# Optimization experiments

Measured on AMD Instinct MI355X. Metric: run time of the kernel, lower is better.

## Reference

```python
import jax, jax.numpy as jnp
import numpy as np

IN_DIM = 256
HIDDEN = 256
N_TAPES = 2
DIM = HIDDEN // N_TAPES          # 128
LSTM_H = 8 * N_TAPES             # 16
SEQ = 256
BATCH = 32
TAPELEN = 256


def setup_inputs() -> dict:
    key = jax.random.key(0)
    ks = jax.random.split(key, 10)
    s = 0.05
    inputs = jax.random.normal(ks[0], (SEQ, BATCH, IN_DIM), jnp.float32)
    # LSTM params (torch gate order: i, f, g, o)
    W_ih = s * jax.random.normal(ks[1], (4 * LSTM_H, IN_DIM), jnp.float32)
    W_hh = s * jax.random.normal(ks[2], (4 * LSTM_H, LSTM_H), jnp.float32)
    b_ih = s * jax.random.normal(ks[3], (4 * LSTM_H,), jnp.float32)
    b_hh = s * jax.random.normal(ks[4], (4 * LSTM_H,), jnp.float32)
    # value / out linear layers
    W_val = s * jax.random.normal(ks[5], (HIDDEN, IN_DIM), jnp.float32)
    b_val = s * jax.random.normal(ks[6], (HIDDEN,), jnp.float32)
    W_out = s * jax.random.normal(ks[7], (HIDDEN, HIDDEN), jnp.float32)
    b_out = s * jax.random.normal(ks[8], (HIDDEN,), jnp.float32)
    return {
        'inputs': inputs, 'tapelen': TAPELEN,
        'W_ih': W_ih, 'W_hh': W_hh, 'b_ih': b_ih, 'b_hh': b_hh,
        'W_val': W_val, 'b_val': b_val, 'W_out': W_out, 'b_out': b_out,
    }


def _lstm(inputs, W_ih, W_hh, b_ih, b_hh):
    # inputs: [S, B, in_dim] -> hidden seq [S, B, LSTM_H], torch gate order i,f,g,o
    S, B, _ = inputs.shape
    xg = inputs @ W_ih.T + (b_ih + b_hh)  # precompute input contribution [S,B,4H]

    def step(carry, xt):
        h, c = carry
        g = xt + h @ W_hh.T
        i, f, gg, o = jnp.split(g, 4, axis=-1)
        c = jax.nn.sigmoid(f) * c + jax.nn.sigmoid(i) * jnp.tanh(gg)
        h = jax.nn.sigmoid(o) * jnp.tanh(c)
        return (h, c), h

    h0 = jnp.zeros((B, W_hh.shape[1]), inputs.dtype)
    (_, _), hs = jax.lax.scan(step, (h0, h0), xg)
    return hs


def reference(inputs, tapelen, W_ih, W_hh, b_ih, b_hh, W_val, b_val, W_out, b_out):
    seqlen, bs, _ = inputs.shape
    values = (inputs @ W_val.T + b_val).reshape(seqlen, bs, N_TAPES, DIM)

    actions = _lstm(inputs, W_ih, W_hh, b_ih, b_hh).reshape(seqlen, bs, N_TAPES, 8)
    dirs_r = jax.nn.softmax(actions[..., 0:3], axis=-1)
    dirs_w = jax.nn.softmax(actions[..., 3:6], axis=-1)
    rwprobs = jax.nn.sigmoid(actions[..., 6:8])

    tape0 = jnp.zeros((tapelen, bs, N_TAPES, DIM), inputs.dtype)
    pos0 = jnp.zeros((tapelen, bs, N_TAPES), inputs.dtype).at[0].set(1.0)

    def step(carry, xs):
        tape, rpos, wpos = carry
        v, rd, wd, rw = xs  # v:[B,T,C] rd/wd:[B,T,3] rw:[B,T,2]
        # write: replace value at soft write position, gated by rw[...,1]
        oldval = jnp.einsum('lntc,lnt->ntc', tape, wpos)
        newmem = jnp.einsum('lnt,ntc->lntc', wpos, v - oldval)
        tape = tape + newmem * rw[None, :, :, 1:2]
        # NOTE: faithful to source — write-position shifts roll rpos, not wpos
        next_w = jnp.roll(rpos, 1, axis=0)
        prev_w = jnp.roll(rpos, -1, axis=0)
        wpos = prev_w * wd[None, :, :, 0] + wpos * wd[None, :, :, 1] + next_w * wd[None, :, :, 2]
        # read, gated by rw[...,0]
        read_out = jnp.einsum('lntc,lnt->ntc', tape, rpos * rw[None, :, :, 0])
        next_r = jnp.roll(rpos, 1, axis=0)
        prev_r = jnp.roll(rpos, -1, axis=0)
        rpos = prev_r * rd[None, :, :, 0] + rpos * rd[None, :, :, 1] + next_r * rd[None, :, :, 2]
        return (tape, rpos, wpos), read_out

    (tape, rpos, wpos), reads = jax.lax.scan(
        step, (tape0, pos0, pos0), (values, dirs_r, dirs_w, rwprobs))

    outputs = reads.reshape(seqlen, bs, HIDDEN) @ W_out.T + b_out
    return outputs, tape, (rpos, wpos)
```

## Files before the change

kernel.cpp:

```cpp
#include <hip/hip_runtime.h>

#define SEQ    256
#define BATCH  32
#define NT     2
#define DIM    128
#define LTAPE  256

typedef float f32x4 __attribute__((ext_vector_type(4)));
typedef short s16x8 __attribute__((ext_vector_type(8)));
typedef unsigned int u32;
typedef unsigned short u16;

__device__ __forceinline__ float sigm(float x) { return 1.f / (1.f + __expf(-x)); }
__device__ __forceinline__ float tanh_(float x) { float e = __expf(2.f * x); return 1.f - 2.f / (e + 1.f); }
__device__ __forceinline__ u16 f2bf(float x) {
  u32 u = __builtin_bit_cast(u32, x);
  u32 r = (u + 0x7fffu + ((u >> 16) & 1u)) >> 16;
  return (u16)r;
}
__device__ __forceinline__ float bf2f(u16 b) {
  u32 u = ((u32)b) << 16; return __builtin_bit_cast(float, u);
}

template<bool A_BF16, bool OUT_BF16>
__global__ __launch_bounds__(256) void gemm_mfma(
    const void* __restrict__ Av, const float* __restrict__ W,
    const float* __restrict__ bias, void* __restrict__ Cv, int N) {
  __shared__ u16 As[128 * 40];
  __shared__ u16 Bs[64 * 40];
  const int tid = threadIdx.x;
  const int bm = blockIdx.x * 128, bn = blockIdx.y * 64;
  const int wv = tid >> 6, lane = tid & 63;
  const int wm = wv >> 1, wn = wv & 1;
  const int l15 = lane & 15, l4 = lane >> 4;
  f32x4 acc[4][2] = {};
  const int arow = tid >> 1, ahalf = tid & 1;
  const int brow = (tid & 127) >> 1, bhalf = tid & 1;

  for (int k0 = 0; k0 < 256; k0 += 32) {
    u16 abuf[16];
    if (A_BF16) {
      const u16* A = (const u16*)Av;
      const uint4* p = (const uint4*)(A + (size_t)(bm + arow) * 256 + k0 + ahalf * 16);
      *(uint4*)(abuf) = p[0]; *(uint4*)(abuf + 8) = p[1];
    } else {
      const float* A = (const float*)Av;
      const float* src = A + (size_t)(bm + arow) * 256 + k0 + ahalf * 16;
      float4 x0 = ((const float4*)src)[0], x1 = ((const float4*)src)[1];
      float4 x2 = ((const float4*)src)[2], x3 = ((const float4*)src)[3];
      float xs[16] = {x0.x, x0.y, x0.z, x0.w, x1.x, x1.y, x1.z, x1.w,
                      x2.x, x2.y, x2.z, x2.w, x3.x, x3.y, x3.z, x3.w};
#pragma unroll
      for (int j = 0; j < 16; ++j) abuf[j] = f2bf(xs[j]);
    }
    u16 bbuf[16];
    if (tid < 128) {
      const float* src = W + (size_t)(bn + brow) * 256 + k0 + bhalf * 16;
      float4 x0 = ((const float4*)src)[0], x1 = ((const float4*)src)[1];
      float4 x2 = ((const float4*)src)[2], x3 = ((const float4*)src)[3];
      float xs[16] = {x0.x, x0.y, x0.z, x0.w, x1.x, x1.y, x1.z, x1.w,
                      x2.x, x2.y, x2.z, x2.w, x3.x, x3.y, x3.z, x3.w};
#pragma unroll
      for (int j = 0; j < 16; ++j) bbuf[j] = f2bf(xs[j]);
    }
    __syncthreads();
    *(uint4*)&As[arow * 40 + ahalf * 16] = *(const uint4*)(abuf);
    *(uint4*)&As[arow * 40 + ahalf * 16 + 8] = *(const uint4*)(abuf + 8);
    if (tid < 128) {
      *(uint4*)&Bs[brow * 40 + bhalf * 16] = *(const uint4*)(bbuf);
      *(uint4*)&Bs[brow * 40 + bhalf * 16 + 8] = *(const uint4*)(bbuf + 8);
    }
    __syncthreads();
    s16x8 af[4], bfr[2];
#pragma unroll
    for (int mi = 0; mi < 4; ++mi)
      af[mi] = *(const s16x8*)&As[(wm * 64 + mi * 16 + l15) * 40 + l4 * 8];
#pragma unroll
    for (int ni = 0; ni < 2; ++ni)
      bfr[ni] = *(const s16x8*)&Bs[(wn * 32 + ni * 16 + l15) * 40 + l4 * 8];
#pragma unroll
    for (int mi = 0; mi < 4; ++mi)
#pragma unroll
      for (int ni = 0; ni < 2; ++ni)
        acc[mi][ni] = __builtin_amdgcn_mfma_f32_16x16x32_bf16(af[mi], bfr[ni], acc[mi][ni], 0, 0, 0);
  }
#pragma unroll
  for (int mi = 0; mi < 4; ++mi)
#pragma unroll
    for (int ni = 0; ni < 2; ++ni)
#pragma unroll
      for (int r = 0; r < 4; ++r) {
        int row = bm + wm * 64 + mi * 16 + l4 * 4 + r;
        int col = bn + wn * 32 + ni * 16 + l15;
        float val = acc[mi][ni][r] + bias[col];
        if (OUT_BF16) ((u16*)Cv)[(size_t)row * N + col] = f2bf(val);
        else          ((float*)Cv)[(size_t)row * N + col] = val;
      }
}

__global__ __launch_bounds__(256) void gemm_nt(
    const float* __restrict__ A, const float* __restrict__ W,
    const float* __restrict__ b1, const float* __restrict__ b2,
    float* __restrict__ C, int N) {
  __shared__ float Asm[16][68];
  __shared__ float Bsm[16][68];
  const int tid = threadIdx.x;
  const int bm = blockIdx.x * 64;
  const int bn = blockIdx.y * 64;
  const int lr = tid >> 2;
  const int lc4 = (tid & 3) * 4;
  const int tm = (tid & 15) * 4;
  const int tn = (tid >> 4) * 4;
  float acc[4][4];
#pragma unroll
  for (int i = 0; i < 4; ++i)
#pragma unroll
    for (int j = 0; j < 4; ++j) acc[i][j] = 0.f;
  for (int k0 = 0; k0 < 256; k0 += 16) {
    float4 av = *reinterpret_cast<const float4*>(&A[(bm + lr) * 256 + k0 + lc4]);
    float4 bv = *reinterpret_cast<const float4*>(&W[(bn + lr) * 256 + k0 + lc4]);
    __syncthreads();
    Asm[lc4 + 0][lr] = av.x; Asm[lc4 + 1][lr] = av.y; Asm[lc4 + 2][lr] = av.z; Asm[lc4 + 3][lr] = av.w;
    Bsm[lc4 + 0][lr] = bv.x; Bsm[lc4 + 1][lr] = bv.y; Bsm[lc4 + 2][lr] = bv.z; Bsm[lc4 + 3][lr] = bv.w;
    __syncthreads();
#pragma unroll
    for (int kk = 0; kk < 16; ++kk) {
      float4 a = *reinterpret_cast<const float4*>(&Asm[kk][tm]);
      float4 b = *reinterpret_cast<const float4*>(&Bsm[kk][tn]);
      float a_[4] = {a.x, a.y, a.z, a.w};
      float b_[4] = {b.x, b.y, b.z, b.w};
#pragma unroll
      for (int i = 0; i < 4; ++i)
#pragma unroll
        for (int j = 0; j < 4; ++j) acc[i][j] += a_[i] * b_[j];
    }
  }
#pragma unroll
  for (int i = 0; i < 4; ++i)
#pragma unroll
    for (int j = 0; j < 4; ++j) {
      int n = bn + tn + j;
      float bias = b1[n] + (b2 ? b2[n] : 0.f);
      C[(size_t)(bm + tm + i) * N + n] = acc[i][j] + bias;
    }
}

__global__ __launch_bounds__(64, 1) void lstm_kernel(
    const float* __restrict__ xg,
    const float* __restrict__ W_hh,
    float* __restrict__ hout) {
  const int lane = threadIdx.x;
  const int b = blockIdx.x;
  const int k = lane & 15, q = lane >> 4;
  float w[16];
#pragma unroll
  for (int kk = 0; kk < 16; ++kk) w[kk] = W_hh[lane * 16 + kk];
  float h = 0.f, c = 0.f;
  const float* xb = xg + (size_t)b * 64 + lane;
  float xA = xb[0 * 2048];
  float xB = xb[1 * 2048];
  float xC = xb[2 * 2048];
  float xD = xb[3 * 2048];

#define LSTM_STEP(S, XV)                                                     \
  {                                                                          \
    float hb[16];                                                            \
    _Pragma("unroll") for (int kk = 0; kk < 16; ++kk)                        \
      hb[kk] = __shfl(h, kk, 64);                                            \
    float pa = w[0] * hb[0], pb = w[1] * hb[1];                              \
    float pcc = w[2] * hb[2], pd = w[3] * hb[3];                             \
    _Pragma("unroll") for (int kk = 4; kk < 16; kk += 4) {                   \
      pa += w[kk + 0] * hb[kk + 0];                                         \
      pb += w[kk + 1] * hb[kk + 1];                                         \
      pcc += w[kk + 2] * hb[kk + 2];                                        \
      pd += w[kk + 3] * hb[kk + 3];                                         \
    }                                                                        \
    float g = XV + (pa + pb) + (pcc + pd);                                   \
    float gi = __shfl(g, k, 64);                                             \
    float gf = __shfl(g, 16 + k, 64);                                        \
    float gg = __shfl(g, 32 + k, 64);                                        \
    float go = __shfl(g, 48 + k, 64);                                        \
    c = sigm(gf) * c + sigm(gi) * tanh_(gg);                                 \
    h = sigm(go) * tanh_(c);                                                 \
    if (q == 0) hout[(size_t)((S) * 32 + b) * 16 + k] = h;                   \
  }

  for (int s0 = 0; s0 < SEQ; s0 += 4) {
    int p4 = s0 + 4; if (p4 > 255) p4 = 255;
    int p5 = s0 + 5; if (p5 > 255) p5 = 255;
    int p6 = s0 + 6; if (p6 > 255) p6 = 255;
    int p7 = s0 + 7; if (p7 > 255) p7 = 255;
    float nA = xb[(size_t)p4 * 2048];
    float nB = xb[(size_t)p5 * 2048];
    float nC = xb[(size_t)p6 * 2048];
    float nD = xb[(size_t)p7 * 2048];
    LSTM_STEP(s0 + 0, xA);
    LSTM_STEP(s0 + 1, xB);
    LSTM_STEP(s0 + 2, xC);
    LSTM_STEP(s0 + 3, xD);
    xA = nA; xB = nB; xC = nC; xD = nD;
  }
#undef LSTM_STEP
}

__global__ __launch_bounds__(256) void head_kernel(
    const float* __restrict__ hout,
    float* __restrict__ pc) {
  const int idx = blockIdx.x * 256 + threadIdx.x;
  const int e = idx & 7, s = (idx >> 3) & 255, p = idx >> 11;
  const int b = p >> 1, t = p & 1;
  const float* hp = hout + ((size_t)(s * 32 + b)) * 16 + t * 8;
  float outv;
  if (e < 3) {
    float a0 = hp[0], a1 = hp[1], a2 = hp[2];
    float m = fmaxf(a0, fmaxf(a1, a2));
    float e0 = __expf(a0 - m), e1 = __expf(a1 - m), e2 = __expf(a2 - m);
    float inv = 1.f / (e0 + e1 + e2);
    outv = (e == 0 ? e0 : (e == 1 ? e1 : e2)) * inv;
  } else if (e < 6) {
    float a3 = hp[3], a4 = hp[4], a5 = hp[5];
    float m = fmaxf(a3, fmaxf(a4, a5));
    float e0 = __expf(a3 - m), e1 = __expf(a4 - m), e2 = __expf(a5 - m);
    float inv = 1.f / (e0 + e1 + e2);
    outv = (e == 3 ? e0 : (e == 4 ? e1 : e2)) * inv;
  } else {
    outv = sigm(hp[e]);
  }
  pc[idx] = outv;
}

__global__ __launch_bounds__(64, 1) void pos_kernel(
    const float* __restrict__ pc,
    float* __restrict__ posW, float* __restrict__ posRs,
    float* __restrict__ out_rpos, float* __restrict__ out_wpos) {
  const int p = blockIdx.x, lane = threadIdx.x;
  float r0 = 0, r1 = 0, r2 = 0, r3 = 0, w0 = 0, w1 = 0, w2 = 0, w3 = 0;
  if (lane == 0) { r0 = 1.f; w0 = 1.f; }
  const float* pcb = pc + (size_t)p * 2048;
  float4 c0 = *(const float4*)&pcb[0];
  float4 c1 = *(const float4*)&pcb[4];
  for (int s0 = 0; s0 < SEQ; s0 += 4) {
    float4 pf[8];
#pragma unroll
    for (int u = 0; u < 4; ++u) {
      int sn = s0 + u + 1; if (sn > 255) sn = 255;
      pf[2 * u]     = *(const float4*)&pcb[sn * 8];
      pf[2 * u + 1] = *(const float4*)&pcb[sn * 8 + 4];
    }
#pragma unroll
    for (int u = 0; u < 4; ++u) {
      const int s = s0 + u;
      size_t ob = ((size_t)p * 256 + s) * 256 + lane * 4;
      *(float4*)(posW + ob) = make_float4(w0, w1, w2, w3);
      float rw0 = c1.z;
      *(float4*)(posRs + ob) = make_float4(r0 * rw0, r1 * rw0, r2 * rw0, r3 * rw0);
      const float crd0 = c0.x, crd1 = c0.y, crd2 = c0.z;
      const float cwd0 = c0.w, cwd1 = c1.x, cwd2 = c1.y;
      float rn  = __shfl(r0, (lane + 1) & 63, 64);
      float rpv = __shfl(r3, (lane + 63) & 63, 64);
      float nw0 = r1 * cwd0 + w0 * cwd1 + rpv * cwd2;
      float nr0 = r1 * crd0 + r0 * crd1 + rpv * crd2;
      float nw1 = r2 * cwd0 + w1 * cwd1 + r0 * cwd2;
      float nr1 = r2 * crd0 + r1 * crd1 + r0 * crd2;
      float nw2 = r3 * cwd0 + w2 * cwd1 + r1 * cwd2;
      float nr2 = r3 * crd0 + r2 * crd1 + r1 * crd2;
      float nw3 = rn * cwd0 + w3 * cwd1 + r2 * cwd2;
      float nr3 = rn * crd0 + r3 * crd1 + r2 * crd2;
      r0 = nr0; r1 = nr1; r2 = nr2; r3 = nr3;
      w0 = nw0; w1 = nw1; w2 = nw2; w3 = nw3;
      c0 = pf[2 * u]; c1 = pf[2 * u + 1];
    }
  }
  out_rpos[(size_t)(lane * 4 + 0) * 64 + p] = r0;
  out_rpos[(size_t)(lane * 4 + 1) * 64 + p] = r1;
  out_rpos[(size_t)(lane * 4 + 2) * 64 + p] = r2;
  out_rpos[(size_t)(lane * 4 + 3) * 64 + p] = r3;
  out_wpos[(size_t)(lane * 4 + 0) * 64 + p] = w0;
  out_wpos[(size_t)(lane * 4 + 1) * 64 + p] = w1;
  out_wpos[(size_t)(lane * 4 + 2) * 64 + p] = w2;
  out_wpos[(size_t)(lane * 4 + 3) * 64 + p] = w3;
}

template<bool TRANS_A, bool B_NT, int MODE, int OUTK, int BROW>
__global__ __launch_bounds__(256) void bgemm(
    const float* __restrict__ A, const float* __restrict__ B,
    const float* __restrict__ pc, float* __restrict__ C,
    size_t sA, size_t sB) {
  __shared__ u16 Ah[128 * 40], Al[128 * 40], Bh[64 * 40], Bl[64 * 40];
  const int p = blockIdx.z;
  const int bm = blockIdx.y * 128, bn = blockIdx.x * 64;
  const int tid = threadIdx.x, wv = tid >> 6, lane = tid & 63;
  const int wm = wv >> 1, wn = wv & 1, l15 = lane & 15, l4 = lane >> 4;
  const int b = p >> 1, t = p & 1;

  if (MODE == 1 && bn >= bm + 128) return;
  if (MODE == 2 && bn >= bm + 128) {
#pragma unroll
    for (int mi = 0; mi < 4; ++mi)
#pragma unroll
      for (int ni = 0; ni < 2; ++ni)
#pragma unroll
        for (int r = 0; r < 4; ++r) {
          int row = bm + wm * 64 + mi * 16 + l4 * 4 + r;
          int col = bn + wn * 32 + ni * 16 + l15;
          C[(size_t)p * 65536 + (size_t)row * 256 + col] = 0.f;
        }
    return;
  }

  const float* Ap = A + (size_t)p * sA;
  const float* Bp = B + (size_t)p * sB;
  f32x4 acc[4][2] = {};

  for (int k0 = 0; k0 < 256; k0 += 32) {
    float xa[16];
    if (!TRANS_A) {
      const int m = tid >> 1, kq = (tid & 1) * 16;
      const float* src = Ap + (size_t)(bm + m) * 256 + k0 + kq;
#pragma unroll
      for (int j = 0; j < 4; ++j) *(float4*)(xa + j * 4) = ((const float4*)src)[j];
    } else {
      const int kr = tid >> 3, mq = (tid & 7) * 16;
      const float* src = Ap + (size_t)(k0 + kr) * 256 + bm + mq;
#pragma unroll
      for (int j = 0; j < 4; ++j) *(float4*)(xa + j * 4) = ((const float4*)src)[j];
    }
    u16 ah[16], al[16];
#pragma unroll
    for (int j = 0; j < 16; ++j) {
      u16 hh = f2bf(xa[j]);
      ah[j] = hh; al[j] = f2bf(xa[j] - bf2f(hh));
    }
    float xb[8];
    if (B_NT) {
      const int n = tid >> 2, kq = (tid & 3) * 8;
      const float* src = Bp + (size_t)(bn + n) * 256 + k0 + kq;
      *(float4*)(xb) = ((const float4*)src)[0];
      *(float4*)(xb + 4) = ((const float4*)src)[1];
    } else {
      const int kr = tid >> 3, nq = (tid & 7) * 8;
      const float* src = Bp + (size_t)(k0 + kr) * BROW + bn + nq;
      *(float4*)(xb) = ((const float4*)src)[0];
      *(float4*)(xb + 4) = ((const float4*)src)[1];
    }
    u16 bh[8], bl[8];
#pragma unroll
    for (int j = 0; j < 8; ++j) {
      u16 hh = f2bf(xb[j]);
      bh[j] = hh; bl[j] = f2bf(xb[j] - bf2f(hh));
    }
    __syncthreads();
    if (!TRANS_A) {
      const int m = tid >> 1, kq = (tid & 1) * 16;
      *(uint4*)&Ah[m * 40 + kq]     = *(const uint4*)(ah);
      *(uint4*)&Ah[m * 40 + kq + 8] = *(const uint4*)(ah + 8);
      *(uint4*)&Al[m * 40 + kq]     = *(const uint4*)(al);
      *(uint4*)&Al[m * 40 + kq + 8] = *(const uint4*)(al + 8);
    } else {
      const int kr = tid >> 3, mq = (tid & 7) * 16;
#pragma unroll
      for (int j = 0; j < 16; ++j) {
        Ah[(mq + j) * 40 + kr] = ah[j];
        Al[(mq + j) * 40 + kr] = al[j];
      }
    }
    if (B_NT) {
      const int n = tid >> 2, kq = (tid & 3) * 8;
      *(uint4*)&Bh[n * 40 + kq] = *(const uint4*)(bh);
      *(uint4*)&Bl[n * 40 + kq] = *(const uint4*)(bl);
    } else {
      const int kr = tid >> 3, nq = (tid & 7) * 8;
#pragma unroll
      for (int j = 0; j < 8; ++j) {
        Bh[(nq + j) * 40 + kr] = bh[j];
        Bl[(nq + j) * 40 + kr] = bl[j];
      }
    }
    __syncthreads();
    s16x8 fah[4], fal[4], fbh[2], fbl[2];
#pragma unroll
    for (int mi = 0; mi < 4; ++mi) {
      fah[mi] = *(const s16x8*)&Ah[(wm * 64 + mi * 16 + l15) * 40 + l4 * 8];
      fal[mi] = *(const s16x8*)&Al[(wm * 64 + mi * 16 + l15) * 40 + l4 * 8];
    }
#pragma unroll
    for (int ni = 0; ni < 2; ++ni) {
      fbh[ni] = *(const s16x8*)&Bh[(wn * 32 + ni * 16 + l15) * 40 + l4 * 8];
      fbl[ni] = *(const s16x8*)&Bl[(wn * 32 + ni * 16 + l15) * 40 + l4 * 8];
    }
#pragma unroll
    for (int mi = 0; mi < 4; ++mi)
#pragma unroll
      for (int ni = 0; ni < 2; ++ni) {
        acc[mi][ni] = __builtin_amdgcn_mfma_f32_16x16x32_bf16(fah[mi], fbh[ni], acc[mi][ni], 0, 0, 0);
        acc[mi][ni] = __builtin_amdgcn_mfma_f32_16x16x32_bf16(fah[mi], fbl[ni], acc[mi][ni], 0, 0, 0);
        acc[mi][ni] = __builtin_amdgcn_mfma_f32_16x16x32_bf16(fal[mi], fbh[ni], acc[mi][ni], 0, 0, 0);
      }
  }
#pragma unroll
  for (int mi = 0; mi < 4; ++mi)
#pragma unroll
    for (int ni = 0; ni < 2; ++ni)
#pragma unroll
      for (int r = 0; r < 4; ++r) {
        int row = bm + wm * 64 + mi * 16 + l4 * 4 + r;
        int col = bn + wn * 32 + ni * 16 + l15;
        float v = acc[mi][ni][r];
        if (MODE == 1) v = (col < row) ? v * pc[((size_t)p * 256 + row) * 8 + 7] : 0.f;
        if (MODE == 2) v = (col <= row) ? v : 0.f;
        if (OUTK == 0)      C[(size_t)p * 65536 + (size_t)row * 256 + col] = v;
        else if (OUTK == 1) C[((size_t)(row * 32 + b)) * 256 + t * 128 + col] = v;
        else                C[((size_t)row * 64 + p) * 128 + col] = v;
      }
}

__global__ __launch_bounds__(64) void inv_kernel(
    const float* __restrict__ L,
    u16* __restrict__ MgH, u16* __restrict__ MgL) {
  const int pk = blockIdx.x;
  const int p = pk >> 3, s0 = (pk & 7) * 32;
  const int lane = threadIdx.x;
  __shared__ float Db[32][33];
  __shared__ float Ms[32][33];
  const float* Lp = L + (size_t)p * 65536;
  {
    const int r = lane >> 1, c0 = (lane & 1) * 16;
    const float* src = Lp + (size_t)(s0 + r) * 256 + s0 + c0;
    float4 v0 = ((const float4*)src)[0], v1 = ((const float4*)src)[1];
    float4 v2 = ((const float4*)src)[2], v3 = ((const float4*)src)[3];
    *(float4*)&Db[r][c0]      = v0; *(float4*)&Db[r][c0 + 4]  = v1;
    *(float4*)&Db[r][c0 + 8]  = v2; *(float4*)&Db[r][c0 + 12] = v3;
  }
  __syncthreads();
  if (lane < 32) {
    const int j = lane;
    float m[32];
#pragma unroll
    for (int r = 0; r < 32; ++r) {
      float xa = (r == j) ? 1.f : 0.f;
      float xb = 0.f;
#pragma unroll
      for (int q = 0; q < 32; ++q) {
        if (q < r) {
          if (q & 1) xb -= Db[r][q] * m[q];
          else       xa -= Db[r][q] * m[q];
        }
      }
      float x = xa + xb;
      m[r] = x;
      Ms[r][j] = x;
    }
  }
  __syncthreads();
  const int l15 = lane & 15, l4 = lane >> 4;
#pragma unroll
  for (int rt = 0; rt < 2; ++rt) {
    u32 wh[4], wl[4];
#pragma unroll
    for (int i2 = 0; i2 < 4; ++i2) {
      float v0 = Ms[rt * 16 + l15][l4 * 8 + i2 * 2];
      float v1 = Ms[rt * 16 + l15][l4 * 8 + i2 * 2 + 1];
      u16 h0 = f2bf(v0), h1 = f2bf(v1);
      u16 g0 = f2bf(v0 - bf2f(h0)), g1 = f2bf(v1 - bf2f(h1));
      wh[i2] = (u32)h0 | ((u32)h1 << 16);
      wl[i2] = (u32)g0 | ((u32)g1 << 16);
    }
    size_t off = (((size_t)pk * 2 + rt) * 64 + lane) * 8;
    *(uint4*)(MgH + off) = make_uint4(wh[0], wh[1], wh[2], wh[3]);
    *(uint4*)(MgL + off) = make_uint4(wl[0], wl[1], wl[2], wl[3]);
  }
}

__global__ __launch_bounds__(256, 1) void solve_kernel(
    const float* __restrict__ L,
    const u16* __restrict__ values,
    const float* __restrict__ pc,
    const u16* __restrict__ MgH, const u16* __restrict__ MgL,
    float* __restrict__ delta) {
  const int p = blockIdx.x >> 1, hf = blockIdx.x & 1;
  const int b = p >> 1, t = p & 1;
  const int tid = threadIdx.x, w = tid >> 6, lane = tid & 63;
  const int l15 = lane & 15, l4 = lane >> 4;
  const int col = w * 16 + l15;
  __shared__ u16 dBsH[64][264];
  __shared__ u16 dBsL[64][264];
  __shared__ u16 Lh[32][264];
  __shared__ u16 Ll[32][264];
  __shared__ u16 accTH[64][40];
  __shared__ u16 accTL[64][40];
  const float* Lp = L + (size_t)p * 65536;
  const int srow = tid >> 3, sseg = tid & 7;

  for (int k = 0; k < 8; ++k) {
    const int s0 = k * 32;
    f32x4 acc0 = {}, acc1 = {};
#pragma unroll
    for (int r = 0; r < 4; ++r) {
      int s = s0 + l4 * 4 + r;
      float rv = bf2f(values[((size_t)(s * 32 + b)) * 256 + t * 128 + hf * 64 + col]);
      acc0[r] = rv * pc[((size_t)p * 256 + s) * 8 + 7];
      int s2 = s + 16;
      float rv2 = bf2f(values[((size_t)(s2 * 32 + b)) * 256 + t * 128 + hf * 64 + col]);
      acc1[r] = rv2 * pc[((size_t)p * 256 + s2) * 8 + 7];
    }
    size_t mo0 = (((size_t)(p * 8 + k) * 2 + 0) * 64 + lane) * 8;
    size_t mo1 = (((size_t)(p * 8 + k) * 2 + 1) * 64 + lane) * 8;
    s16x8 mh0 = *(const s16x8*)(MgH + mo0);
    s16x8 mh1 = *(const s16x8*)(MgH + mo1);
    s16x8 ml0 = *(const s16x8*)(MgL + mo0);
    s16x8 ml1 = *(const s16x8*)(MgL + mo1);
    for (int c4 = sseg; c4 * 4 < s0; c4 += 8) {
      float4 lv = *(const float4*)(Lp + (size_t)(s0 + srow) * 256 + c4 * 4);
      float x0 = -lv.x, x1 = -lv.y, x2 = -lv.z, x3 = -lv.w;
      u16 h0 = f2bf(x0), h1 = f2bf(x1), h2 = f2bf(x2), h3 = f2bf(x3);
      u16 g0 = f2bf(x0 - bf2f(h0)), g1 = f2bf(x1 - bf2f(h1));
      u16 g2 = f2bf(x2 - bf2f(h2)), g3 = f2bf(x3 - bf2f(h3));
      *(uint2*)&Lh[srow][c4 * 4] = make_uint2((u32)h0 | ((u32)h1 << 16), (u32)h2 | ((u32)h3 << 16));
      *(uint2*)&Ll[srow][c4 * 4] = make_uint2((u32)g0 | ((u32)g1 << 16), (u32)g2 | ((u32)g3 << 16));
    }
    __syncthreads();
    for (int m = 0; m < k; ++m) {
      s16x8 bh = *(const s16x8*)&dBsH[col][m * 32 + l4 * 8];
      s16x8 bl = *(const s16x8*)&dBsL[col][m * 32 + l4 * 8];
      s16x8 a0h = *(const s16x8*)&Lh[l15][m * 32 + l4 * 8];
      s16x8 a0l = *(const s16x8*)&Ll[l15][m * 32 + l4 * 8];
      s16x8 a1h = *(const s16x8*)&Lh[16 + l15][m * 32 + l4 * 8];
      s16x8 a1l = *(const s16x8*)&Ll[16 + l15][m * 32 + l4 * 8];
      acc0 = __builtin_amdgcn_mfma_f32_16x16x32_bf16(a0h, bh, acc0, 0, 0, 0);
      acc0 = __builtin_amdgcn_mfma_f32_16x16x32_bf16(a0h, bl, acc0, 0, 0, 0);
      acc0 = __builtin_amdgcn_mfma_f32_16x16x32_bf16(a0l, bh, acc0, 0, 0, 0);
      acc1 = __builtin_amdgcn_mfma_f32_16x16x32_bf16(a1h, bh, acc1, 0, 0, 0);
      acc1 = __builtin_amdgcn_mfma_f32_16x16x32_bf16(a1h, bl, acc1, 0, 0, 0);
      acc1 = __builtin_amdgcn_mfma_f32_16x16x32_bf16(a1l, bh, acc1, 0, 0, 0);
    }
    {
      u16 th[8], tl[8];
#pragma unroll
      for (int r = 0; r < 4; ++r) {
        u16 h = f2bf(acc0[r]); th[r] = h; tl[r] = f2bf(acc0[r] - bf2f(h));
        u16 h2 = f2bf(acc1[r]); th[4 + r] = h2; tl[4 + r] = f2bf(acc1[r] - bf2f(h2));
      }
      *(uint2*)&accTH[col][l4 * 4]      = make_uint2((u32)th[0] | ((u32)th[1] << 16), (u32)th[2] | ((u32)th[3] << 16));
      *(uint2*)&accTH[col][16 + l4 * 4] = make_uint2((u32)th[4] | ((u32)th[5] << 16), (u32)th[6] | ((u32)th[7] << 16));
      *(uint2*)&accTL[col][l4 * 4]      = make_uint2((u32)tl[0] | ((u32)tl[1] << 16), (u32)tl[2] | ((u32)tl[3] << 16));
      *(uint2*)&accTL[col][16 + l4 * 4] = make_uint2((u32)tl[4] | ((u32)tl[5] << 16), (u32)tl[6] | ((u32)tl[7] << 16));
    }
    f32x4 d0 = {}, d1 = {};
    {
      s16x8 bh = *(const s16x8*)&accTH[col][l4 * 8];
      s16x8 bl = *(const s16x8*)&accTL[col][l4 * 8];
      d0 = __builtin_amdgcn_mfma_f32_16x16x32_bf16(mh0, bh, d0, 0, 0, 0);
      d0 = __builtin_amdgcn_mfma_f32_16x16x32_bf16(mh0, bl, d0, 0, 0, 0);
      d0 = __builtin_amdgcn_mfma_f32_16x16x32_bf16(ml0, bh, d0, 0, 0, 0);
      d1 = __builtin_amdgcn_mfma_f32_16x16x32_bf16(mh1, bh, d1, 0, 0, 0);
      d1 = __builtin_amdgcn_mfma_f32_16x16x32_bf16(mh1, bl, d1, 0, 0, 0);
      d1 = __builtin_amdgcn_mfma_f32_16x16x32_bf16(ml1, bh, d1, 0, 0, 0);
    }
#pragma unroll
    for (int r = 0; r < 4; ++r) {
      int row0 = l4 * 4 + r;
      delta[((size_t)p * 256 + s0 + row0) * 128 + hf * 64 + col] = d0[r];
      delta[((size_t)p * 256 + s0 + 16 + row0) * 128 + hf * 64 + col] = d1[r];
    }
    {
      u16 dh[8], dl[8];
#pragma unroll
      for (int r = 0; r < 4; ++r) {
        u16 h = f2bf(d0[r]); dh[r] = h; dl[r] = f2bf(d0[r] - bf2f(h));
        u16 h2 = f2bf(d1[r]); dh[4 + r] = h2; dl[4 + r] = f2bf(d1[r] - bf2f(h2));
      }
      *(uint2*)&dBsH[col][s0 + l4 * 4]      = make_uint2((u32)dh[0] | ((u32)dh[1] << 16), (u32)dh[2] | ((u32)dh[3] << 16));
      *(uint2*)&dBsH[col][s0 + 16 + l4 * 4] = make_uint2((u32)dh[4] | ((u32)dh[5] << 16), (u32)dh[6] | ((u32)dh[7] << 16));
      *(uint2*)&dBsL[col][s0 + l4 * 4]      = make_uint2((u32)dl[0] | ((u32)dl[1] << 16), (u32)dl[2] | ((u32)dl[3] << 16));
      *(uint2*)&dBsL[col][s0 + 16 + l4 * 4] = make_uint2((u32)dl[4] | ((u32)dl[5] << 16), (u32)dl[6] | ((u32)dl[7] << 16));
    }
    __syncthreads();
  }
}

extern "C" void kernel_launch(void* const* d_in, const int* in_sizes, int n_in,
                              void* d_out, int out_size, void* d_ws, size_t ws_size,
                              hipStream_t stream) {
  const float* inputs = (const float*)d_in[0];
  const float* W_ih = (const float*)d_in[2];
  const float* W_hh = (const float*)d_in[3];
  const float* b_ih = (const float*)d_in[4];
  const float* b_hh = (const float*)d_in[5];
  const float* W_val = (const float*)d_in[6];
  const float* b_val = (const float*)d_in[7];
  const float* W_out = (const float*)d_in[8];
  const float* b_out = (const float*)d_in[9];

  float* out = (float*)d_out;
  float* out_tape = out + 2097152;
  float* out_rpos = out + 4194304;
  float* out_wpos = out + 4210688;

  char* ws = (char*)d_ws;
  float* posW      = (float*)(ws);
  float* posRs     = (float*)(ws + 16777216);
  float* LHm       = (float*)(ws + 33554432);
  u16*   values_bf = (u16*)  (ws + 50331648);
  float* xg        = (float*)(ws + 54525952);
  float* delta     = (float*)(ws + 54525952);
  float* pcb       = (float*)(ws + 62914560);
  float* hout      = (float*)(ws + 63438848);
  u16*   MgH       = (u16*)  (ws + 63963136);
  u16*   MgL       = (u16*)  (ws + 65011712);
  float* reads_f32 = posRs;

  gemm_mfma<false, true><<<dim3(64, 4), 256, 0, stream>>>(inputs, W_val, b_val, values_bf, 256);
  gemm_nt<<<dim3(128, 1), 256, 0, stream>>>(inputs, W_ih, b_ih, b_hh, xg, 64);
  lstm_kernel<<<32, 64, 0, stream>>>(xg, W_hh, hout);
  head_kernel<<<512, 256, 0, stream>>>(hout, pcb);
  pos_kernel<<<64, 64, 0, stream>>>(pcb, posW, posRs, out_rpos, out_wpos);
  bgemm<false, true, 1, 0, 256><<<dim3(4, 2, 64), 256, 0, stream>>>(
      posW, posW, pcb, LHm, 65536, 65536);
  inv_kernel<<<512, 64, 0, stream>>>(LHm, MgH, MgL);
  solve_kernel<<<128, 256, 0, stream>>>(LHm, values_bf, pcb, MgH, MgL, delta);
  bgemm<false, true, 2, 0, 256><<<dim3(4, 2, 64), 256, 0, stream>>>(
      posRs, posW, pcb, LHm, 65536, 65536);
  bgemm<false, false, 0, 1, 128><<<dim3(2, 2, 64), 256, 0, stream>>>(
      LHm, delta, pcb, reads_f32, 65536, 32768);
  bgemm<true, false, 0, 2, 128><<<dim3(2, 2, 64), 256, 0, stream>>>(
      posW, delta, pcb, out_tape, 65536, 32768);
  gemm_mfma<false, false><<<dim3(64, 4), 256, 0, stream>>>(reads_f32, W_out, b_out, out, 256);
}
```

Measured before the change: 380.8 us.

## Pack four batches per LSTM wavefront with gate-interleaved input projection layout

The input-projection GEMM now writes its gate columns permuted so that each hidden unit's four gates (i,f,g,o) sit next to each other. This lets each LSTM lane load them as one float4 and compute all four gate dot products itself. Each 64-lane wavefront now handles four batch elements (16 lanes each), which removes the per-step gate shuffles and cuts the LSTM launch from 32 blocks to 8. The cost is four times more FMA work per lane on the serial recurrence, 64 weight registers per lane, and fewer CUs in use.

New measurement: 382.1 us. Within noise of the previous version (+0.3%).

```diff
diff --git a/kernel.cpp b/kernel.cpp
--- a/kernel.cpp
+++ b/kernel.cpp
@@ -98,6 +98,7 @@
       }
 }
 
+template<bool PERM>
 __global__ __launch_bounds__(256) void gemm_nt(
     const float* __restrict__ A, const float* __restrict__ W,
     const float* __restrict__ b1, const float* __restrict__ b2,
@@ -116,9 +117,11 @@
   for (int i = 0; i < 4; ++i)
 #pragma unroll
     for (int j = 0; j < 4; ++j) acc[i][j] = 0.f;
+  int wr = bn + lr;
+  if (PERM) wr = ((wr & 3) * 16) + (wr >> 2);
   for (int k0 = 0; k0 < 256; k0 += 16) {
     float4 av = *reinterpret_cast<const float4*>(&A[(bm + lr) * 256 + k0 + lc4]);
-    float4 bv = *reinterpret_cast<const float4*>(&W[(bn + lr) * 256 + k0 + lc4]);
+    float4 bv = *reinterpret_cast<const float4*>(&W[wr * 256 + k0 + lc4]);
     __syncthreads();
     Asm[lc4 + 0][lr] = av.x; Asm[lc4 + 1][lr] = av.y; Asm[lc4 + 2][lr] = av.z; Asm[lc4 + 3][lr] = av.w;
     Bsm[lc4 + 0][lr] = bv.x; Bsm[lc4 + 1][lr] = bv.y; Bsm[lc4 + 2][lr] = bv.z; Bsm[lc4 + 3][lr] = bv.w;
@@ -140,7 +143,8 @@
 #pragma unroll
     for (int j = 0; j < 4; ++j) {
       int n = bn + tn + j;
-      float bias = b1[n] + (b2 ? b2[n] : 0.f);
+      int jm = PERM ? ((n & 3) * 16) + (n >> 2) : n;
+      float bias = b1[jm] + (b2 ? b2[jm] : 0.f);
       C[(size_t)(bm + tm + i) * N + n] = acc[i][j] + bias;
     }
 }
@@ -150,39 +154,52 @@
     const float* __restrict__ W_hh,
     float* __restrict__ hout) {
   const int lane = threadIdx.x;
-  const int b = blockIdx.x;
-  const int k = lane & 15, q = lane >> 4;
-  float w[16];
-#pragma unroll
-  for (int kk = 0; kk < 16; ++kk) w[kk] = W_hh[lane * 16 + kk];
+  const int b4 = lane >> 4, k = lane & 15;
+  const int b = blockIdx.x * 4 + b4;
+  const int lbase = lane & 48;
+  float w[4][16];
+#pragma unroll
+  for (int q = 0; q < 4; ++q)
+#pragma unroll
+    for (int kk = 0; kk < 16; ++kk)
+      w[q][kk] = W_hh[(q * 16 + k) * 16 + kk];
+#pragma unroll
+  for (int q = 0; q < 4; ++q)
+#pragma unroll
+    for (int kk = 0; kk < 16; ++kk)
+      asm volatile("" : "+v"(w[q][kk]));
+
   float h = 0.f, c = 0.f;
-  const float* xb = xg + (size_t)b * 64 + lane;
-  float xA = xb[0 * 2048];
-  float xB = xb[1 * 2048];
-  float xC = xb[2 * 2048];
-  float xD = xb[3 * 2048];
+  const float* xb = xg + (size_t)b * 64 + k * 4;
+  float4 xA = *(const float4*)(xb + (size_t)0 * 2048);
+  float4 xB = *(const float4*)(xb + (size_t)1 * 2048);
+  float4 xC = *(const float4*)(xb + (size_t)2 * 2048);
+  float4 xD = *(const float4*)(xb + (size_t)3 * 2048);
 
 #define LSTM_STEP(S, XV)                                                     \
   {                                                                          \
     float hb[16];                                                            \
     _Pragma("unroll") for (int kk = 0; kk < 16; ++kk)                        \
-      hb[kk] = __shfl(h, kk, 64);                                            \
-    float pa = w[0] * hb[0], pb = w[1] * hb[1];                              \
-    float pcc = w[2] * hb[2], pd = w[3] * hb[3];                             \
-    _Pragma("unroll") for (int kk = 4; kk < 16; kk += 4) {                   \
-      pa += w[kk + 0] * hb[kk + 0];                                         \
-      pb += w[kk + 1] * hb[kk + 1];                                         \
-      pcc += w[kk + 2] * hb[kk + 2];                                        \
-      pd += w[kk + 3] * hb[kk + 3];                                         \
+      hb[kk] = __shfl(h, lbase + kk, 64);                                    \
+    float g0, g1, g2, g3;                                                    \
+    _Pragma("unroll") for (int q = 0; q < 4; ++q) {                          \
+      float pa = w[q][0] * hb[0], pb = w[q][1] * hb[1];                      \
+      float pc_ = w[q][2] * hb[2], pd = w[q][3] * hb[3];                     \
+      _Pragma("unroll") for (int kk = 4; kk < 16; kk += 4) {                 \
+        pa += w[q][kk + 0] * hb[kk + 0];                                     \
+        pb += w[q][kk + 1] * hb[kk + 1];                                     \
+        pc_ += w[q][kk + 2] * hb[kk + 2];                                    \
+        pd += w[q][kk + 3] * hb[kk + 3];                                     \
+      }                                                                      \
+      float r = (pa + pb) + (pc_ + pd);                                      \
+      if (q == 0) g0 = XV.x + r;                                             \
+      else if (q == 1) g1 = XV.y + r;                                        \
+      else if (q == 2) g2 = XV.z + r;                                        \
+      else g3 = XV.w + r;                                                    \
     }                                                                        \
-    float g = XV + (pa + pb) + (pcc + pd);                                   \
-    float gi = __shfl(g, k, 64);                                             \
-    float gf = __shfl(g, 16 + k, 64);                                        \
-    float gg = __shfl(g, 32 + k, 64);                                        \
-    float go = __shfl(g, 48 + k, 64);                                        \
-    c = sigm(gf) * c + sigm(gi) * tanh_(gg);                                 \
-    h = sigm(go) * tanh_(c);                                                 \
-    if (q == 0) hout[(size_t)((S) * 32 + b) * 16 + k] = h;                   \
+    c = sigm(g1) * c + sigm(g0) * tanh_(g2);                                 \
+    h = sigm(g3) * tanh_(c);                                                 \
+    hout[(size_t)(S) * 512 + blockIdx.x * 64 + lane] = h;                    \
   }
 
   for (int s0 = 0; s0 < SEQ; s0 += 4) {
@@ -190,10 +207,10 @@
     int p5 = s0 + 5; if (p5 > 255) p5 = 255;
     int p6 = s0 + 6; if (p6 > 255) p6 = 255;
     int p7 = s0 + 7; if (p7 > 255) p7 = 255;
-    float nA = xb[(size_t)p4 * 2048];
-    float nB = xb[(size_t)p5 * 2048];
-    float nC = xb[(size_t)p6 * 2048];
-    float nD = xb[(size_t)p7 * 2048];
+    float4 nA = *(const float4*)(xb + (size_t)p4 * 2048);
+    float4 nB = *(const float4*)(xb + (size_t)p5 * 2048);
+    float4 nC = *(const float4*)(xb + (size_t)p6 * 2048);
+    float4 nD = *(const float4*)(xb + (size_t)p7 * 2048);
     LSTM_STEP(s0 + 0, xA);
     LSTM_STEP(s0 + 1, xB);
     LSTM_STEP(s0 + 2, xC);
@@ -610,8 +627,8 @@
   float* reads_f32 = posRs;
 
   gemm_mfma<false, true><<<dim3(64, 4), 256, 0, stream>>>(inputs, W_val, b_val, values_bf, 256);
-  gemm_nt<<<dim3(128, 1), 256, 0, stream>>>(inputs, W_ih, b_ih, b_hh, xg, 64);
-  lstm_kernel<<<32, 64, 0, stream>>>(xg, W_hh, hout);
+  gemm_nt<true><<<dim3(128, 1), 256, 0, stream>>>(inputs, W_ih, b_ih, b_hh, xg, 64);
+  lstm_kernel<<<8, 64, 0, stream>>>(xg, W_hh, hout);
   head_kernel<<<512, 256, 0, stream>>>(hout, pcb);
   pos_kernel<<<64, 64, 0, stream>>>(pcb, posW, posRs, out_rpos, out_wpos);
   bgemm<false, true, 1, 0, 256><<<dim3(4, 2, 64), 256, 0, stream>>>(
```
